# Kernel tuning notes

Hardware: AMD Instinct MI355X
Metric: run time of the kernel (lower is better)

## Reference

```python
import jax, jax.numpy as jnp
import numpy as np

N_NODES, N_EDGES, N_GRAPHS = 50000, 800000, 512
F_IN, HID, DIM_OUT = 128, 256, 16


def setup_inputs() -> dict:
    key = jax.random.key(0)
    ks = jax.random.split(key, 16)
    glorot = lambda k, fi, fo: jax.random.normal(k, (fi, fo), jnp.float32) * jnp.sqrt(2.0 / (fi + fo))
    return {
        "x": jax.random.normal(ks[0], (N_NODES, F_IN), jnp.float32),
        "edge_index": jax.random.randint(ks[1], (2, N_EDGES), 0, N_NODES, dtype=jnp.int32),
        "batch": jnp.sort(jax.random.randint(ks[2], (N_NODES,), 0, N_GRAPHS, dtype=jnp.int32)),
        "mol_wt": jax.random.uniform(ks[3], (N_GRAPHS, 1), jnp.float32),
        "n_rings": jax.random.uniform(ks[4], (N_GRAPHS, 1), jnp.float32),
        "W1": glorot(ks[5], F_IN, HID), "b1": jnp.zeros((HID,), jnp.float32),
        "W2": glorot(ks[6], HID, HID), "b2": jnp.zeros((HID,), jnp.float32),
        "W3": glorot(ks[7], HID, HID), "b3": jnp.zeros((HID,), jnp.float32),
        "fcW1": glorot(ks[8], HID + 2, 196), "fcb1": jnp.zeros((196,), jnp.float32),
        "fcW2": glorot(ks[9], 196, DIM_OUT), "fcb2": jnp.zeros((DIM_OUT,), jnp.float32),
    }


def _gcn_conv(x, W, b, src, dst, deg_inv_sqrt, n_nodes):
    # PyG GCNConv: linear transform, then D^-1/2 (A+I) D^-1/2 aggregation, then bias
    xw = x @ W  # [N, HID]
    norm = deg_inv_sqrt[src] * deg_inv_sqrt[dst]  # [E+N]
    msg = norm[:, None] * xw[src]  # gather + scale
    out = jax.ops.segment_sum(msg, dst, num_segments=n_nodes)  # scatter-add at targets
    return out + b


def reference(x, edge_index, batch, mol_wt, n_rings,
              W1, b1, W2, b2, W3, b3, fcW1, fcb1, fcW2, fcb2):
    n_nodes = x.shape[0]
    self_loop = jnp.arange(n_nodes, dtype=edge_index.dtype)
    src = jnp.concatenate([edge_index[0], self_loop])
    dst = jnp.concatenate([edge_index[1], self_loop])
    deg = jax.ops.segment_sum(jnp.ones_like(dst, dtype=x.dtype), dst, num_segments=n_nodes)
    deg_inv_sqrt = jnp.where(deg > 0, jax.lax.rsqrt(deg), 0.0)

    h = jax.nn.relu(_gcn_conv(x, W1, b1, src, dst, deg_inv_sqrt, n_nodes))
    h = jax.nn.relu(_gcn_conv(h, W2, b2, src, dst, deg_inv_sqrt, n_nodes))
    h = jax.nn.relu(_gcn_conv(h, W3, b3, src, dst, deg_inv_sqrt, n_nodes))

    n_graphs = mol_wt.shape[0]
    sums = jax.ops.segment_sum(h, batch, num_segments=n_graphs)
    counts = jax.ops.segment_sum(jnp.ones((n_nodes,), h.dtype), batch, num_segments=n_graphs)
    hg = sums / jnp.maximum(counts, 1.0)[:, None]  # global mean pool

    hg = jnp.concatenate([hg, mol_wt, n_rings], axis=1)  # [G, 258]
    hg = jax.nn.relu(hg @ fcW1 + fcb1)
    return hg @ fcW2 + fcb2
```

## Files before the change

### kernel.cpp

```cpp
#include <hip/hip_runtime.h>

#define NN 50000
#define NE 800000
#define NG 512
#define FIN 128
#define HID 256
#define NBUK 196
#define SEGSZ 2048

typedef short short8 __attribute__((ext_vector_type(8)));
typedef float f32x4 __attribute__((ext_vector_type(4)));
typedef float f32x2 __attribute__((ext_vector_type(2)));
typedef unsigned short u16x8 __attribute__((ext_vector_type(8)));
typedef unsigned int u32x2 __attribute__((ext_vector_type(2)));
typedef unsigned int u32x4 __attribute__((ext_vector_type(4)));

static inline int cdiv(int a, int b) { return (a + b - 1) / b; }

static __device__ inline unsigned short f2bf(float f) {
    unsigned int u = __float_as_uint(f);
    unsigned int r = (u + 0x7FFF + ((u >> 16) & 1)) >> 16;
    return (unsigned short)r;
}
static __device__ inline float bf2f(unsigned short h) {
    return __uint_as_float(((unsigned int)h) << 16);
}
static __device__ inline float bflo(unsigned int p) { return __uint_as_float(p << 16); }
static __device__ inline float bfhi(unsigned int p) { return __uint_as_float(p & 0xFFFF0000u); }

static __device__ __forceinline__ f32x2 pkadd(f32x2 a, f32x2 b) {
    f32x2 r;
    asm("v_pk_add_f32 %0, %1, %2" : "=v"(r) : "v"(a), "v"(b));
    return r;
}

template <int J>
static __device__ __forceinline__ int bswz(int v) {
    return __builtin_amdgcn_ds_swizzle(v, (J << 5) | 0x18);
}

typedef __attribute__((address_space(1))) unsigned int gu32;
typedef __attribute__((address_space(3))) unsigned int lu32;
static __device__ __forceinline__ void gload16(const unsigned short* g, unsigned short* l) {
    __builtin_amdgcn_global_load_lds((const gu32*)(const void*)g, (lu32*)(void*)l, 16, 0, 0);
}


__global__ __launch_bounds__(256) void hist_bucket_kernel(const int* __restrict__ dst,
                                                          int* __restrict__ gbuk) {
    __shared__ int lh[NBUK];
    int tid = threadIdx.x;
    for (int j = tid; j < NBUK; j += 256) lh[j] = 0;
    __syncthreads();
    int base = blockIdx.x * 2048;
    #pragma unroll
    for (int k = 0; k < 8; ++k) {
        int i = base + k * 256 + tid;
        if (i < NE) atomicAdd(&lh[dst[i] >> 8], 1);
    }
    __syncthreads();
    for (int j = tid; j < NBUK; j += 256) if (lh[j]) atomicAdd(&gbuk[j], lh[j]);
}

__global__ void goff_kernel(const int* __restrict__ batch, int* __restrict__ goff) {
    int i = blockIdx.x * 256 + threadIdx.x;
    if (i >= NN) return;
    int b = batch[i];
    int pb = (i == 0) ? -1 : batch[i - 1];
    for (int g = pb + 1; g <= b; ++g) goff[g] = i;
    if (i == NN - 1) for (int g = b + 1; g <= NG; ++g) goff[g] = NN;
}

__global__ void buk_scan_kernel(const int* __restrict__ gbuk, int* __restrict__ bukoff,
                                int* __restrict__ bukcur) {
    __shared__ int ws[4];
    int tid = threadIdx.x, lane = tid & 63, wid = tid >> 6;
    int v = (tid < NBUK) ? gbuk[tid] : 0;
    int incl = v;
    #pragma unroll
    for (int off = 1; off < 64; off <<= 1) {
        int u = __shfl_up(incl, off, 64);
        if (lane >= off) incl += u;
    }
    if (lane == 63) ws[wid] = incl;
    __syncthreads();
    int woff = 0;
    for (int w = 0; w < wid; ++w) woff += ws[w];
    int ex = woff + incl - v;
    if (tid < NBUK) { bukoff[tid] = ex; bukcur[tid] = ex; }
    if (tid == NBUK - 1) bukoff[NBUK] = ex + v;
}

__global__ __launch_bounds__(256) void scatter_kernel(const int* __restrict__ src,
                                                      const int* __restrict__ dst,
                                                      int* __restrict__ bukcur,
                                                      unsigned int* __restrict__ pairs) {
    __shared__ int lh[NBUK];
    __shared__ int lbase[NBUK];
    int tid = threadIdx.x;
    for (int j = tid; j < NBUK; j += 256) lh[j] = 0;
    __syncthreads();
    int base = blockIdx.x * 2048;
    int d[8], s[8];
    #pragma unroll
    for (int k = 0; k < 8; ++k) {
        int i = base + k * 256 + tid;
        if (i < NE) {
            d[k] = dst[i]; s[k] = src[i];
            atomicAdd(&lh[d[k] >> 8], 1);
        } else d[k] = -1;
    }
    __syncthreads();
    for (int j = tid; j < NBUK; j += 256) lbase[j] = lh[j] ? atomicAdd(&bukcur[j], lh[j]) : 0;
    __syncthreads();
    for (int j = tid; j < NBUK; j += 256) lh[j] = 0;
    __syncthreads();
    #pragma unroll
    for (int k = 0; k < 8; ++k) {
        if (d[k] >= 0) {
            int b = d[k] >> 8;
            int loc = atomicAdd(&lh[b], 1);
            pairs[lbase[b] + loc] = ((unsigned int)s[k] << 16) | (unsigned int)(d[k] & 255);
        }
    }
}

__global__ __launch_bounds__(256) void local_csr_kernel(const unsigned int* __restrict__ pairs,
                                                        const int* __restrict__ bukoff,
                                                        int* __restrict__ row_ptr,
                                                        int* __restrict__ col8,
                                                        float* __restrict__ dis) {
    __shared__ int fcnt[256];
    __shared__ int foff[256];
    __shared__ int fws[4];
    int b = blockIdx.x, tid = threadIdx.x;
    int beg = bukoff[b], end = bukoff[b + 1];
    fcnt[tid] = 0;
    __syncthreads();
    for (int i = beg + tid; i < end; i += 256) atomicAdd(&fcnt[pairs[i] & 255], 1);
    __syncthreads();
    int lane = tid & 63, wid = tid >> 6;
    int v = fcnt[tid], incl = v;
    #pragma unroll
    for (int off = 1; off < 64; off <<= 1) {
        int u = __shfl_up(incl, off, 64);
        if (lane >= off) incl += u;
    }
    if (lane == 63) fws[wid] = incl;
    __syncthreads();
    int woff = 0;
    for (int w = 0; w < wid; ++w) woff += fws[w];
    int ex = woff + incl - v;
    foff[tid] = ex;
    int gid = b * 256 + tid;
    if (gid < NN) {
        row_ptr[gid] = beg + ex;
        dis[gid] = rsqrtf((float)v + 1.0f);
    }
    if (b == 0 && tid == 0) row_ptr[NN] = NE;
    __syncthreads();
    for (int i = beg + tid; i < end; i += 256) {
        unsigned int p = pairs[i];
        int loc = atomicAdd(&foff[p & 255], 1);
        col8[beg + loc] = (int)(p >> 16) << 3;
    }
}

__global__ __launch_bounds__(256) void segperm_kernel(const int* __restrict__ row_ptr,
                                                      const float* __restrict__ dis,
                                                      u32x4* __restrict__ desc) {
    __shared__ int hist[256];
    __shared__ int ws[4];
    int tid = threadIdx.x;
    int base = blockIdx.x * SEGSZ;
    int segN = NN - base; if (segN > SEGSZ) segN = SEGSZ;
    hist[tid] = 0;
    __syncthreads();
    int dbin[8], rb[8], dreal[8];
    #pragma unroll
    for (int k = 0; k < 8; ++k) {
        int j = k * 256 + tid;
        if (j < segN) {
            rb[k] = row_ptr[base + j];
            dreal[k] = row_ptr[base + j + 1] - rb[k];
            int d = dreal[k] > 255 ? 255 : dreal[k];
            dbin[k] = d;
            atomicAdd(&hist[d], 1);
        } else dbin[k] = -1;
    }
    __syncthreads();
    int lane = tid & 63, wid = tid >> 6;
    int v = hist[tid], incl = v;
    #pragma unroll
    for (int off = 1; off < 64; off <<= 1) {
        int u = __shfl_up(incl, off, 64);
        if (lane >= off) incl += u;
    }
    if (lane == 63) ws[wid] = incl;
    __syncthreads();
    int woff = 0;
    for (int w = 0; w < wid; ++w) woff += ws[w];
    __syncthreads();
    hist[tid] = woff + incl - v;
    __syncthreads();
    #pragma unroll
    for (int k = 0; k < 8; ++k) {
        if (dbin[k] >= 0) {
            int rank = atomicAdd(&hist[dbin[k]], 1);
            int node = base + k * 256 + tid;
            u32x4 dd;
            dd.x = (unsigned int)(node * 8);
            dd.y = (unsigned int)rb[k];
            dd.z = (unsigned int)(rb[k] + dreal[k]);
            dd.w = __float_as_uint(dis[node]);
            desc[base + rank] = dd;
        }
    }
}

__global__ void cast_scale_kernel(const float* __restrict__ x, const float* __restrict__ dis,
                                  unsigned short* __restrict__ Xb, int n4) {
    int i = blockIdx.x * 256 + threadIdx.x;
    if (i < n4) {
        int node = i >> 5;
        int f4 = i & 31;
        int s = f4 >> 3;
        int o = f4 & 7;
        float dv = dis[node];
        float4 v = ((const float4*)x)[i];
        ushort4 w;
        w.x = f2bf(dv * v.x); w.y = f2bf(dv * v.y); w.z = f2bf(dv * v.z); w.w = f2bf(dv * v.w);
        ((ushort4*)Xb)[((size_t)s * NN + (size_t)node) * 8 + o] = w;
    }
}

__global__ void tcast_all_kernel(const float* __restrict__ W1, const float* __restrict__ W2,
                                 const float* __restrict__ W3,
                                 unsigned short* __restrict__ W1t, unsigned short* __restrict__ W2t,
                                 unsigned short* __restrict__ W3t) {
    int idx = blockIdx.x * 256 + threadIdx.x;
    if (idx < FIN * 256) {
        int n = idx / FIN, k = idx - n * FIN;
        W1t[idx] = f2bf(W1[(size_t)k * 256 + n]);
    } else if (idx < FIN * 256 + HID * 256) {
        int t = idx - FIN * 256;
        int n = t / HID, k = t - n * HID;
        W2t[t] = f2bf(W2[(size_t)k * 256 + n]);
    } else {
        int t = idx - FIN * 256 - HID * 256;
        int n = t / HID, k = t - n * HID;
        W3t[t] = f2bf(W3[(size_t)k * 256 + n]);
    }
}

#define CLD 136
template <int MODE>
__global__ __launch_bounds__(256) void gemm128_kernel(
        const unsigned short* __restrict__ A, const unsigned short* __restrict__ Bt,
        const float* __restrict__ dis, const float* __restrict__ bias,
        unsigned short* __restrict__ Cout, int M, int K) {
    __shared__ unsigned short smem[128 * CLD];
    unsigned short* As = smem;
    unsigned short* Bs = smem + 4096;
    const int tid = threadIdx.x;
    const int bm = blockIdx.x * 128, bn = blockIdx.y * 128;
    const int wave = tid >> 6, lane = tid & 63;
    const int l16 = lane & 15, quad = lane >> 4;
    const int wm = (wave & 1) * 64, wn = (wave >> 1) * 64;

    int srow0 = tid >> 2, skc = (tid & 3) * 8;
    int srow1 = (256 + tid) >> 2;
    int ar0 = bm + srow0; if (ar0 > M - 1) ar0 = M - 1;
    int ar1 = bm + srow1; if (ar1 > M - 1) ar1 = M - 1;

    f32x4 acc[4][4];
    #pragma unroll
    for (int i = 0; i < 4; ++i)
        #pragma unroll
        for (int j = 0; j < 4; ++j) acc[i][j] = (f32x4){0.f, 0.f, 0.f, 0.f};

    for (int k0 = 0; k0 < K; k0 += 32) {
        gload16(A + (size_t)ar0 * K + k0 + skc, &As[(size_t)tid * 8]);
        gload16(A + (size_t)ar1 * K + k0 + skc, &As[(size_t)(256 + tid) * 8]);
        gload16(Bt + (size_t)(bn + srow0) * K + k0 + skc, &Bs[(size_t)tid * 8]);
        gload16(Bt + (size_t)(bn + srow1) * K + k0 + skc, &Bs[(size_t)(256 + tid) * 8]);
        __syncthreads();
        short8 af[4], bf[4];
        #pragma unroll
        for (int mt = 0; mt < 4; ++mt) af[mt] = *(const short8*)&As[(wm + mt * 16 + l16) * 32 + quad * 8];
        #pragma unroll
        for (int nt = 0; nt < 4; ++nt) bf[nt] = *(const short8*)&Bs[(wn + nt * 16 + l16) * 32 + quad * 8];
        #pragma unroll
        for (int mt = 0; mt < 4; ++mt)
            #pragma unroll
            for (int nt = 0; nt < 4; ++nt)
                acc[mt][nt] = __builtin_amdgcn_mfma_f32_16x16x32_bf16(af[mt], bf[nt], acc[mt][nt], 0, 0, 0);
        __syncthreads();
    }
    float bv[4];
    #pragma unroll
    for (int nt = 0; nt < 4; ++nt) bv[nt] = bias[bn + wn + nt * 16 + l16];
    #pragma unroll
    for (int mt = 0; mt < 4; ++mt) {
        #pragma unroll
        for (int r = 0; r < 4; ++r) {
            int lrow = wm + mt * 16 + quad * 4 + r;
            int grow = bm + lrow; if (grow > M - 1) grow = M - 1;
            float dv = (MODE == 0) ? dis[grow] : 1.0f;
            #pragma unroll
            for (int nt = 0; nt < 4; ++nt) {
                float v = fmaxf(acc[mt][nt][r] + bv[nt], 0.f);
                if (MODE == 0) v *= dv;
                smem[lrow * CLD + wn + nt * 16 + l16] = f2bf(v);
            }
        }
    }
    __syncthreads();
    for (int c = tid; c < 2048; c += 256) {
        int lrow = c >> 4, coff = (c & 15) << 3;
        int grow = bm + lrow;
        if (grow < M) {
            if (MODE == 0) {
                int gcol = bn + coff;
                int s = gcol >> 5, o = gcol & 31;
                *(u16x8*)(Cout + ((size_t)s * M + (size_t)grow) * 32 + o) =
                    *(const u16x8*)&smem[lrow * CLD + coff];
            } else {
                *(u16x8*)(Cout + (size_t)grow * HID + bn + coff) =
                    *(const u16x8*)&smem[lrow * CLD + coff];
            }
        }
    }
}
#undef CLD

template <int S>
__global__ __launch_bounds__(256) void agg_slice_kernel(
        const unsigned short* __restrict__ Hb, const u32x4* __restrict__ desc,
        const int* __restrict__ col8,
        unsigned short* __restrict__ Out, int n, int nchunk) {
    constexpr int LOGS = (S == 8) ? 3 : 2;
    int bid = blockIdx.x;
    int s = bid & (S - 1);
    int chunk = nchunk - 1 - (bid >> LOGS);
    int idx = chunk * 32 + (threadIdx.x >> 3);
    if (idx >= n) return;
    int lane8 = threadIdx.x & 7;
    u32x4 d = desc[idx];
    int node8 = (int)d.x;
    int e = (int)d.y, eend = (int)d.z;
    float dv = __uint_as_float(d.w);
    const u32x2* Hv = (const u32x2*)Hb + (size_t)s * NN * 8;
    u32x2 p = Hv[node8 + lane8];
    f32x2 a01 = {bflo(p.x), bfhi(p.x)};
    f32x2 a23 = {bflo(p.y), bfhi(p.y)};

    for (; e + 16 <= eend; e += 16) {
        int cv0 = col8[e + lane8];
        int cv1 = col8[e + 8 + lane8];
        u32x2 m[16];
#define G0(J) m[J] = Hv[bswz<J>(cv0) + lane8];
#define G1(J) m[8 + J] = Hv[bswz<J>(cv1) + lane8];
        G0(0) G0(1) G0(2) G0(3) G0(4) G0(5) G0(6) G0(7)
        G1(0) G1(1) G1(2) G1(3) G1(4) G1(5) G1(6) G1(7)
#undef G0
#undef G1
        #pragma unroll
        for (int j = 0; j < 16; ++j) {
            f32x2 lo = {bflo(m[j].x), bfhi(m[j].x)};
            f32x2 hi = {bflo(m[j].y), bfhi(m[j].y)};
            a01 = pkadd(a01, lo);
            a23 = pkadd(a23, hi);
        }
    }
    if (e + 8 <= eend) {
        int cv0 = col8[e + lane8];
        u32x2 m[8];
#define G0(J) m[J] = Hv[bswz<J>(cv0) + lane8];
        G0(0) G0(1) G0(2) G0(3) G0(4) G0(5) G0(6) G0(7)
#undef G0
        #pragma unroll
        for (int j = 0; j < 8; ++j) {
            f32x2 lo = {bflo(m[j].x), bfhi(m[j].x)};
            f32x2 hi = {bflo(m[j].y), bfhi(m[j].y)};
            a01 = pkadd(a01, lo);
            a23 = pkadd(a23, hi);
        }
        e += 8;
    }
    int t = eend - e;
    if (t > 0) {
        int il = e + lane8; if (il >= eend) il = eend - 1;
        int cv0 = col8[il];
        u32x2 m[7];
#define GT(J) if (J < t) m[J] = Hv[bswz<J>(cv0) + lane8];
        GT(0) GT(1) GT(2) GT(3) GT(4) GT(5) GT(6)
#undef GT
#define AT(J) if (J < t) { f32x2 lo = {bflo(m[J].x), bfhi(m[J].x)}; \
                           f32x2 hi = {bflo(m[J].y), bfhi(m[J].y)}; \
                           a01 = pkadd(a01, lo); a23 = pkadd(a23, hi); }
        AT(0) AT(1) AT(2) AT(3) AT(4) AT(5) AT(6)
#undef AT
    }
    int node = node8 >> 3;
    u32x2 o;
    o.x = (unsigned int)f2bf(dv * a01.x) | ((unsigned int)f2bf(dv * a01.y) << 16);
    o.y = (unsigned int)f2bf(dv * a23.x) | ((unsigned int)f2bf(dv * a23.y) << 16);
    __builtin_nontemporal_store(o, (u32x2*)Out + (size_t)node * (S * 8) + s * 8 + lane8);
}

__global__ __launch_bounds__(256) void pool_part_kernel(
        const unsigned short* __restrict__ H, const int* __restrict__ goff,
        float* __restrict__ part) {
    __shared__ float red[3][64][4];
    int bid = blockIdx.x;
    int g = bid >> 2, q = bid & 3;
    int beg = goff[g], end = goff[g + 1];
    int len = end - beg;
    int qb = beg + ((len * q) >> 2), qe = beg + ((len * (q + 1)) >> 2);
    int tp = threadIdx.x >> 6, tf = threadIdx.x & 63;
    float4 acc = make_float4(0.f, 0.f, 0.f, 0.f);
    int i = qb + tp;
    for (; i + 12 < qe; i += 16) {
        ushort4 v0 = *(const ushort4*)&H[(size_t)(i     ) * HID + tf * 4];
        ushort4 v1 = *(const ushort4*)&H[(size_t)(i +  4) * HID + tf * 4];
        ushort4 v2 = *(const ushort4*)&H[(size_t)(i +  8) * HID + tf * 4];
        ushort4 v3 = *(const ushort4*)&H[(size_t)(i + 12) * HID + tf * 4];
        acc.x += bf2f(v0.x) + bf2f(v1.x) + bf2f(v2.x) + bf2f(v3.x);
        acc.y += bf2f(v0.y) + bf2f(v1.y) + bf2f(v2.y) + bf2f(v3.y);
        acc.z += bf2f(v0.z) + bf2f(v1.z) + bf2f(v2.z) + bf2f(v3.z);
        acc.w += bf2f(v0.w) + bf2f(v1.w) + bf2f(v2.w) + bf2f(v3.w);
    }
    for (; i < qe; i += 4) {
        ushort4 v = *(const ushort4*)&H[(size_t)i * HID + tf * 4];
        acc.x += bf2f(v.x); acc.y += bf2f(v.y); acc.z += bf2f(v.z); acc.w += bf2f(v.w);
    }
    if (tp > 0) {
        red[tp - 1][tf][0] = acc.x; red[tp - 1][tf][1] = acc.y;
        red[tp - 1][tf][2] = acc.z; red[tp - 1][tf][3] = acc.w;
    }
    __syncthreads();
    if (tp == 0) {
        acc.x += red[0][tf][0] + red[1][tf][0] + red[2][tf][0];
        acc.y += red[0][tf][1] + red[1][tf][1] + red[2][tf][1];
        acc.z += red[0][tf][2] + red[1][tf][2] + red[2][tf][2];
        acc.w += red[0][tf][3] + red[1][tf][3] + red[2][tf][3];
        ((float4*)part)[(size_t)bid * 64 + tf] = acc;
    }
}

__global__ __launch_bounds__(256) void mlp_kernel(
        const float* __restrict__ part, const int* __restrict__ goff,
        const float* __restrict__ mol, const float* __restrict__ rings,
        const float* __restrict__ fcW1, const float* __restrict__ fcb1,
        const float* __restrict__ fcW2, const float* __restrict__ fcb2,
        float* __restrict__ out) {
    __shared__ float s_hg[258];
    __shared__ float s_t[196];
    __shared__ float s_p[16][16];
    int g = blockIdx.x, tid = threadIdx.x;
    int len = goff[g + 1] - goff[g];
    const float* pg = part + (size_t)g * 1024;
    float v = pg[tid] + pg[256 + tid] + pg[512 + tid] + pg[768 + tid];
    s_hg[tid] = v / fmaxf((float)len, 1.0f);
    if (tid == 0) { s_hg[256] = mol[g]; s_hg[257] = rings[g]; }
    __syncthreads();
    if (tid < 196) {
        float a = fcb1[tid];
        int k = 0;
        for (; k + 8 <= 258; k += 8) {
            float w0 = fcW1[(k + 0) * 196 + tid];
            float w1 = fcW1[(k + 1) * 196 + tid];
            float w2 = fcW1[(k + 2) * 196 + tid];
            float w3 = fcW1[(k + 3) * 196 + tid];
            float w4 = fcW1[(k + 4) * 196 + tid];
            float w5 = fcW1[(k + 5) * 196 + tid];
            float w6 = fcW1[(k + 6) * 196 + tid];
            float w7 = fcW1[(k + 7) * 196 + tid];
            a = fmaf(s_hg[k + 0], w0, a); a = fmaf(s_hg[k + 1], w1, a);
            a = fmaf(s_hg[k + 2], w2, a); a = fmaf(s_hg[k + 3], w3, a);
            a = fmaf(s_hg[k + 4], w4, a); a = fmaf(s_hg[k + 5], w5, a);
            a = fmaf(s_hg[k + 6], w6, a); a = fmaf(s_hg[k + 7], w7, a);
        }
        for (; k < 258; ++k) a = fmaf(s_hg[k], fcW1[k * 196 + tid], a);
        s_t[tid] = fmaxf(a, 0.f);
    }
    __syncthreads();
    {
        int o = tid & 15, kp = tid >> 4;
        float a = 0.f;
        for (int k = kp; k < 196; k += 16) a = fmaf(s_t[k], fcW2[k * 16 + o], a);
        s_p[kp][o] = a;
    }
    __syncthreads();
    if (tid < 16) {
        float a = fcb2[tid];
        #pragma unroll
        for (int kp = 0; kp < 16; ++kp) a += s_p[kp][tid];
        out[g * 16 + tid] = a;
    }
}

extern "C" void kernel_launch(void* const* d_in, const int* in_sizes, int n_in,
                              void* d_out, int out_size, void* d_ws, size_t ws_size,
                              hipStream_t stream) {
    const float* x     = (const float*)d_in[0];
    const int*   ei    = (const int*)d_in[1];
    const int*   batch = (const int*)d_in[2];
    const float* mol   = (const float*)d_in[3];
    const float* rings = (const float*)d_in[4];
    const float* W1 = (const float*)d_in[5];
    const float* b1 = (const float*)d_in[6];
    const float* W2 = (const float*)d_in[7];
    const float* b2 = (const float*)d_in[8];
    const float* W3 = (const float*)d_in[9];
    const float* b3 = (const float*)d_in[10];
    const float* fcW1 = (const float*)d_in[11];
    const float* fcb1 = (const float*)d_in[12];
    const float* fcW2 = (const float*)d_in[13];
    const float* fcb2 = (const float*)d_in[14];
    float* out = (float*)d_out;
    const int* src = ei;
    const int* dst = ei + NE;

    char* w = (char*)d_ws;
    auto alloc = [&](size_t bytes) {
        char* p = w;
        w += (bytes + 255) & ~(size_t)255;
        return p;
    };
    int*   gbuk    = (int*)alloc((size_t)NBUK * 4);
    int*   bukoff  = (int*)alloc((size_t)(NBUK + 1) * 4);
    int*   bukcur  = (int*)alloc((size_t)NBUK * 4);
    int*   row_ptr = (int*)alloc((size_t)(NN + 1) * 4);
    int*   goff    = (int*)alloc((size_t)(NG + 1) * 4);
    float* dis     = (float*)alloc((size_t)NN * 4);
    u32x4* desc    = (u32x4*)alloc((size_t)NN * 16);
    unsigned int* pairs = (unsigned int*)alloc((size_t)NE * 4);
    int*   col8    = (int*)alloc((size_t)NE * 4);
    float* part    = (float*)alloc((size_t)NG * 4 * 256 * 4);
    unsigned short* Xs  = (unsigned short*)alloc((size_t)NN * FIN * 2);
    unsigned short* Xa  = (unsigned short*)alloc((size_t)NN * FIN * 2);
    unsigned short* Hs  = (unsigned short*)alloc((size_t)NN * HID * 2);
    unsigned short* Ga  = (unsigned short*)alloc((size_t)NN * HID * 2);
    unsigned short* Hf  = (unsigned short*)alloc((size_t)NN * HID * 2);
    unsigned short* W1t = (unsigned short*)alloc((size_t)FIN * HID * 2);
    unsigned short* W2t = (unsigned short*)alloc((size_t)HID * HID * 2);
    unsigned short* W3t = (unsigned short*)alloc((size_t)HID * HID * 2);

    hipMemsetAsync(gbuk, 0, (size_t)NBUK * 4, stream);
    int eb = cdiv(NE, 2048);
    hist_bucket_kernel<<<eb, 256, 0, stream>>>(dst, gbuk);
    goff_kernel<<<cdiv(NN, 256), 256, 0, stream>>>(batch, goff);
    buk_scan_kernel<<<1, 256, 0, stream>>>(gbuk, bukoff, bukcur);
    scatter_kernel<<<eb, 256, 0, stream>>>(src, dst, bukcur, pairs);
    local_csr_kernel<<<NBUK, 256, 0, stream>>>(pairs, bukoff, row_ptr, col8, dis);
    segperm_kernel<<<cdiv(NN, SEGSZ), 256, 0, stream>>>(row_ptr, dis, desc);

    cast_scale_kernel<<<cdiv(NN * FIN / 4, 256), 256, 0, stream>>>(x, dis, Xs, NN * FIN / 4);
    tcast_all_kernel<<<cdiv((FIN + HID + HID) * 256, 256), 256, 0, stream>>>(W1, W2, W3, W1t, W2t, W3t);

    dim3 ggrid(cdiv(NN, 128), 2);
    int achunks = cdiv(NN, 32);
    agg_slice_kernel<4><<<4 * achunks, 256, 0, stream>>>(Xs, desc, col8, Xa, NN, achunks);
    gemm128_kernel<0><<<ggrid, 256, 0, stream>>>(Xa, W1t, dis, b1, Hs, NN, FIN);
    agg_slice_kernel<8><<<8 * achunks, 256, 0, stream>>>(Hs, desc, col8, Ga, NN, achunks);
    gemm128_kernel<0><<<ggrid, 256, 0, stream>>>(Ga, W2t, dis, b2, Hs, NN, HID);
    agg_slice_kernel<8><<<8 * achunks, 256, 0, stream>>>(Hs, desc, col8, Ga, NN, achunks);
    gemm128_kernel<1><<<ggrid, 256, 0, stream>>>(Ga, W3t, dis, b3, Hf, NN, HID);
    pool_part_kernel<<<NG * 4, 256, 0, stream>>>(Hf, goff, part);
    mlp_kernel<<<NG, 256, 0, stream>>>(part, goff, mol, rings, fcW1, fcb1, fcW2, fcb2, out);
}
```

Before: 351.3 us.

## Widen feature slices from 32 to 64 columns with 16 lanes per node

Changes the sliced feature layout so each slice holds 64 bf16 columns instead of 32. The layout is used by the input cast, the GEMM epilogue and the aggregation kernels, and the node and column descriptors are rescaled to match. Each aggregation group now uses 16 lanes per node, sharing column indices via 16-lane swizzles, and there are half as many slices. Gathers become 128-byte rows per neighbor, meant to improve memory transaction efficiency. The trade-off is coarser tail handling (up to 15 leftover edges) and fewer slices to parallelise across.

```diff
diff --git a/kernel.cpp b/kernel.cpp
--- a/kernel.cpp
+++ b/kernel.cpp
@@ -35,8 +35,8 @@
 }
 
 template <int J>
-static __device__ __forceinline__ int bswz(int v) {
-    return __builtin_amdgcn_ds_swizzle(v, (J << 5) | 0x18);
+static __device__ __forceinline__ int bswz16(int v) {
+    return __builtin_amdgcn_ds_swizzle(v, (J << 5) | 0x10);
 }
 
 typedef __attribute__((address_space(1))) unsigned int gu32;
@@ -128,7 +128,7 @@
 __global__ __launch_bounds__(256) void local_csr_kernel(const unsigned int* __restrict__ pairs,
                                                         const int* __restrict__ bukoff,
                                                         int* __restrict__ row_ptr,
-                                                        int* __restrict__ col8,
+                                                        int* __restrict__ col16,
                                                         float* __restrict__ dis) {
     __shared__ int fcnt[256];
     __shared__ int foff[256];
@@ -162,7 +162,7 @@
     for (int i = beg + tid; i < end; i += 256) {
         unsigned int p = pairs[i];
         int loc = atomicAdd(&foff[p & 255], 1);
-        col8[beg + loc] = (int)(p >> 16) << 3;
+        col16[beg + loc] = (int)(p >> 16) << 4;
     }
 }
 
@@ -209,7 +209,7 @@
             int rank = atomicAdd(&hist[dbin[k]], 1);
             int node = base + k * 256 + tid;
             u32x4 dd;
-            dd.x = (unsigned int)(node * 8);
+            dd.x = (unsigned int)node;
             dd.y = (unsigned int)rb[k];
             dd.z = (unsigned int)(rb[k] + dreal[k]);
             dd.w = __float_as_uint(dis[node]);
@@ -224,13 +224,13 @@
     if (i < n4) {
         int node = i >> 5;
         int f4 = i & 31;
-        int s = f4 >> 3;
-        int o = f4 & 7;
+        int s = f4 >> 4;
+        int o = f4 & 15;
         float dv = dis[node];
         float4 v = ((const float4*)x)[i];
         ushort4 w;
         w.x = f2bf(dv * v.x); w.y = f2bf(dv * v.y); w.z = f2bf(dv * v.z); w.w = f2bf(dv * v.w);
-        ((ushort4*)Xb)[((size_t)s * NN + (size_t)node) * 8 + o] = w;
+        ((ushort4*)Xb)[((size_t)s * NN + (size_t)node) * 16 + o] = w;
     }
 }
 
@@ -322,8 +322,8 @@
         if (grow < M) {
             if (MODE == 0) {
                 int gcol = bn + coff;
-                int s = gcol >> 5, o = gcol & 31;
-                *(u16x8*)(Cout + ((size_t)s * M + (size_t)grow) * 32 + o) =
+                int s = gcol >> 6, o = gcol & 63;
+                *(u16x8*)(Cout + ((size_t)s * M + (size_t)grow) * 64 + o) =
                     *(const u16x8*)&smem[lrow * CLD + coff];
             } else {
                 *(u16x8*)(Cout + (size_t)grow * HID + bn + coff) =
@@ -337,34 +337,31 @@
 template <int S>
 __global__ __launch_bounds__(256) void agg_slice_kernel(
         const unsigned short* __restrict__ Hb, const u32x4* __restrict__ desc,
-        const int* __restrict__ col8,
+        const int* __restrict__ col16,
         unsigned short* __restrict__ Out, int n, int nchunk) {
-    constexpr int LOGS = (S == 8) ? 3 : 2;
+    constexpr int LOGS = (S == 4) ? 2 : 1;
     int bid = blockIdx.x;
     int s = bid & (S - 1);
     int chunk = nchunk - 1 - (bid >> LOGS);
-    int idx = chunk * 32 + (threadIdx.x >> 3);
+    int idx = chunk * 16 + (threadIdx.x >> 4);
     if (idx >= n) return;
-    int lane8 = threadIdx.x & 7;
+    int lane16 = threadIdx.x & 15;
     u32x4 d = desc[idx];
-    int node8 = (int)d.x;
+    int node = (int)d.x;
     int e = (int)d.y, eend = (int)d.z;
     float dv = __uint_as_float(d.w);
-    const u32x2* Hv = (const u32x2*)Hb + (size_t)s * NN * 8;
-    u32x2 p = Hv[node8 + lane8];
+    const u32x2* Hv = (const u32x2*)Hb + (size_t)s * NN * 16;
+    u32x2 p = Hv[node * 16 + lane16];
     f32x2 a01 = {bflo(p.x), bfhi(p.x)};
     f32x2 a23 = {bflo(p.y), bfhi(p.y)};
 
     for (; e + 16 <= eend; e += 16) {
-        int cv0 = col8[e + lane8];
-        int cv1 = col8[e + 8 + lane8];
+        int cv = col16[e + lane16];
         u32x2 m[16];
-#define G0(J) m[J] = Hv[bswz<J>(cv0) + lane8];
-#define G1(J) m[8 + J] = Hv[bswz<J>(cv1) + lane8];
+#define G0(J) m[J] = Hv[bswz16<J>(cv) + lane16];
         G0(0) G0(1) G0(2) G0(3) G0(4) G0(5) G0(6) G0(7)
-        G1(0) G1(1) G1(2) G1(3) G1(4) G1(5) G1(6) G1(7)
+        G0(8) G0(9) G0(10) G0(11) G0(12) G0(13) G0(14) G0(15)
 #undef G0
-#undef G1
         #pragma unroll
         for (int j = 0; j < 16; ++j) {
             f32x2 lo = {bflo(m[j].x), bfhi(m[j].x)};
@@ -373,40 +370,26 @@
             a23 = pkadd(a23, hi);
         }
     }
-    if (e + 8 <= eend) {
-        int cv0 = col8[e + lane8];
-        u32x2 m[8];
-#define G0(J) m[J] = Hv[bswz<J>(cv0) + lane8];
-        G0(0) G0(1) G0(2) G0(3) G0(4) G0(5) G0(6) G0(7)
-#undef G0
-        #pragma unroll
-        for (int j = 0; j < 8; ++j) {
-            f32x2 lo = {bflo(m[j].x), bfhi(m[j].x)};
-            f32x2 hi = {bflo(m[j].y), bfhi(m[j].y)};
-            a01 = pkadd(a01, lo);
-            a23 = pkadd(a23, hi);
-        }
-        e += 8;
-    }
     int t = eend - e;
     if (t > 0) {
-        int il = e + lane8; if (il >= eend) il = eend - 1;
-        int cv0 = col8[il];
-        u32x2 m[7];
-#define GT(J) if (J < t) m[J] = Hv[bswz<J>(cv0) + lane8];
-        GT(0) GT(1) GT(2) GT(3) GT(4) GT(5) GT(6)
+        int il = e + lane16; if (il >= eend) il = eend - 1;
+        int cv = col16[il];
+        u32x2 m[15];
+#define GT(J) if (J < t) m[J] = Hv[bswz16<J>(cv) + lane16];
+        GT(0) GT(1) GT(2) GT(3) GT(4) GT(5) GT(6) GT(7)
+        GT(8) GT(9) GT(10) GT(11) GT(12) GT(13) GT(14)
 #undef GT
 #define AT(J) if (J < t) { f32x2 lo = {bflo(m[J].x), bfhi(m[J].x)}; \
                            f32x2 hi = {bflo(m[J].y), bfhi(m[J].y)}; \
                            a01 = pkadd(a01, lo); a23 = pkadd(a23, hi); }
-        AT(0) AT(1) AT(2) AT(3) AT(4) AT(5) AT(6)
+        AT(0) AT(1) AT(2) AT(3) AT(4) AT(5) AT(6) AT(7)
+        AT(8) AT(9) AT(10) AT(11) AT(12) AT(13) AT(14)
 #undef AT
     }
-    int node = node8 >> 3;
     u32x2 o;
     o.x = (unsigned int)f2bf(dv * a01.x) | ((unsigned int)f2bf(dv * a01.y) << 16);
     o.y = (unsigned int)f2bf(dv * a23.x) | ((unsigned int)f2bf(dv * a23.y) << 16);
-    __builtin_nontemporal_store(o, (u32x2*)Out + (size_t)node * (S * 8) + s * 8 + lane8);
+    __builtin_nontemporal_store(o, (u32x2*)Out + (size_t)node * (S * 16) + s * 16 + lane16);
 }
 
 __global__ __launch_bounds__(256) void pool_part_kernel(
@@ -537,7 +520,7 @@
     float* dis     = (float*)alloc((size_t)NN * 4);
     u32x4* desc    = (u32x4*)alloc((size_t)NN * 16);
     unsigned int* pairs = (unsigned int*)alloc((size_t)NE * 4);
-    int*   col8    = (int*)alloc((size_t)NE * 4);
+    int*   col16   = (int*)alloc((size_t)NE * 4);
     float* part    = (float*)alloc((size_t)NG * 4 * 256 * 4);
     unsigned short* Xs  = (unsigned short*)alloc((size_t)NN * FIN * 2);
     unsigned short* Xa  = (unsigned short*)alloc((size_t)NN * FIN * 2);
@@ -554,19 +537,19 @@
     goff_kernel<<<cdiv(NN, 256), 256, 0, stream>>>(batch, goff);
     buk_scan_kernel<<<1, 256, 0, stream>>>(gbuk, bukoff, bukcur);
     scatter_kernel<<<eb, 256, 0, stream>>>(src, dst, bukcur, pairs);
-    local_csr_kernel<<<NBUK, 256, 0, stream>>>(pairs, bukoff, row_ptr, col8, dis);
+    local_csr_kernel<<<NBUK, 256, 0, stream>>>(pairs, bukoff, row_ptr, col16, dis);
     segperm_kernel<<<cdiv(NN, SEGSZ), 256, 0, stream>>>(row_ptr, dis, desc);
 
     cast_scale_kernel<<<cdiv(NN * FIN / 4, 256), 256, 0, stream>>>(x, dis, Xs, NN * FIN / 4);
     tcast_all_kernel<<<cdiv((FIN + HID + HID) * 256, 256), 256, 0, stream>>>(W1, W2, W3, W1t, W2t, W3t);
 
     dim3 ggrid(cdiv(NN, 128), 2);
-    int achunks = cdiv(NN, 32);
-    agg_slice_kernel<4><<<4 * achunks, 256, 0, stream>>>(Xs, desc, col8, Xa, NN, achunks);
+    int achunks = cdiv(NN, 16);
+    agg_slice_kernel<2><<<2 * achunks, 256, 0, stream>>>(Xs, desc, col16, Xa, NN, achunks);
     gemm128_kernel<0><<<ggrid, 256, 0, stream>>>(Xa, W1t, dis, b1, Hs, NN, FIN);
-    agg_slice_kernel<8><<<8 * achunks, 256, 0, stream>>>(Hs, desc, col8, Ga, NN, achunks);
+    agg_slice_kernel<4><<<4 * achunks, 256, 0, stream>>>(Hs, desc, col16, Ga, NN, achunks);
     gemm128_kernel<0><<<ggrid, 256, 0, stream>>>(Ga, W2t, dis, b2, Hs, NN, HID);
-    agg_slice_kernel<8><<<8 * achunks, 256, 0, stream>>>(Hs, desc, col8, Ga, NN, achunks);
+    agg_slice_kernel<4><<<4 * achunks, 256, 0, stream>>>(Hs, desc, col16, Ga, NN, achunks);
     gemm128_kernel<1><<<ggrid, 256, 0, stream>>>(Ga, W3t, dis, b3, Hf, NN, HID);
     pool_part_kernel<<<NG * 4, 256, 0, stream>>>(Hf, goff, part);
     mlp_kernel<<<NG, 256, 0, stream>>>(part, goff, mol, rings, fcW1, fcb1, fcW2, fcb2, out);
```

Measured after the change: 333.7 us. 1.05x faster.
